# Optimization experiments

Hardware: AMD Instinct MI355X
Metric: run time of the kernel (lower is better)

The kernel has to match this reference:

```python
import jax, jax.numpy as jnp
import numpy as np

ALPHA, BETA, GAMMA = 8.0, 16.0, 16.0  # module defaults


def setup_inputs() -> dict:
    key = jax.random.key(0)
    ks = jax.random.split(key, 8)
    B, T, C = 8, 2048, 128
    d_half, d_rff, lmax, S = 128, 256, 64, 4
    x = jax.random.normal(ks[0], (B, T, C), dtype=jnp.float32)
    # RFF buffers: W ~ N(0,1)/sqrt(c), b ~ U(0, 2pi)
    W = jax.random.normal(ks[1], (C, d_half), dtype=jnp.float32) / np.sqrt(C).astype(np.float32)
    b = 2.0 * np.pi * jax.random.uniform(ks[2], (d_half,), dtype=jnp.float32)
    # phi = Linear(d_rff -> c) + Tanh
    lim = 1.0 / np.sqrt(d_rff)
    phi_w = jax.random.uniform(ks[3], (d_rff, C), minval=-lim, maxval=lim, dtype=jnp.float32)
    phi_b = jax.random.uniform(ks[4], (C,), minval=-lim, maxval=lim, dtype=jnp.float32)
    # anchor is zero-init in torch; use small randn so it contributes
    anchor = 0.02 * jax.random.normal(ks[5], (S, C), dtype=jnp.float32)
    # log-length priors: log_w[s, L-1] = -L / 2^s
    lengths = jnp.arange(1, lmax + 1, dtype=jnp.float32)
    log_w = jnp.stack([-lengths / (2.0 ** s) for s in range(S)])
    lim2 = 1.0 / np.sqrt(S * C)
    mix_w = jax.random.uniform(ks[6], (S * C, C), minval=-lim2, maxval=lim2, dtype=jnp.float32)
    mix_b = jax.random.uniform(ks[7], (C,), minval=-lim2, maxval=lim2, dtype=jnp.float32)
    return {"x": x, "W": W, "b": b, "phi_w": phi_w, "phi_b": phi_b,
            "anchor": anchor, "log_w": log_w, "mix_w": mix_w, "mix_b": mix_b}


def _forward(x, W, b, phi_w, phi_b, anchor, log_w, mix_w, mix_b):
    B, T, C = x.shape
    d_half = W.shape[1]
    d_rff = 2 * d_half
    S, lmax = log_w.shape
    # random Fourier features and causal prefix sums
    z = x @ W + b                                   # (B,T,d_half)
    u = jnp.concatenate([jnp.cos(z), jnp.sin(z)], -1) * (1.0 / np.sqrt(d_half).astype(np.float32))
    pref = jnp.concatenate([jnp.zeros((B, 1, d_rff), x.dtype), jnp.cumsum(u, axis=1)], 1)  # (B,T+1,d)
    # front-pad by lmax so window gathers never go out of bounds
    pref_pad = jnp.concatenate([jnp.zeros((B, lmax, d_rff), x.dtype), pref], 1)            # (B,T+1+lmax,d)

    lengths = jnp.arange(1, lmax + 1, dtype=x.dtype)
    neg_inf = jnp.float32(-jnp.inf)
    # rolling buffers hold states logZ/q/k at indices t-lmax..t-1 (ascending);
    # -inf logZ at out-of-range slots masks invalid segment lengths exactly like L=min(t,lmax)
    logZ0 = jnp.full((S, B, lmax), neg_inf).at[:, :, -1].set(0.0)  # logZ[0]=0
    q0 = jnp.zeros((S, B, lmax, C), x.dtype)
    k0 = jnp.zeros((S, B, lmax), x.dtype)

    @jax.checkpoint
    def step(carry, t):
        logZ_buf, q_buf, k_buf = carry
        # pref[t-lmax .. t]  (pad offset lmax -> start index t)
        sl = jax.lax.dynamic_slice(pref_pad, (0, t, 0), (B, lmax + 1, d_rff))
        # starts = t - lengths, lengths = 1..lmax  -> reversed leading window
        seg_sum = sl[:, -1][:, None, :] - sl[:, :-1][:, ::-1, :]          # (B,lmax,d)
        seg_mean = seg_sum / (lengths + ALPHA)[None, :, None]
        seg_emb = jnp.tanh(seg_mean @ phi_w + phi_b)                      # (B,lmax,C)
        loga = log_w[:, None, :] + logZ_buf[:, :, ::-1]                   # (S,B,lmax)
        pi = jax.nn.softmax(loga, axis=-1)
        q_t = jnp.einsum('sbl,sblc->sbc', pi, q_buf[:, :, ::-1, :] + seg_emb[None])
        k_t = jnp.sum(pi * (k_buf[:, :, ::-1] + 1.0), axis=-1)            # (S,B)
        logZ_t = jax.scipy.special.logsumexp(loga, axis=-1)               # (S,B)
        carry = (jnp.concatenate([logZ_buf[:, :, 1:], logZ_t[:, :, None]], -1),
                 jnp.concatenate([q_buf[:, :, 1:], q_t[:, :, None, :]], 2),
                 jnp.concatenate([k_buf[:, :, 1:], k_t[:, :, None]], -1))
        return carry, (q_t, k_t)

    _, (qs, ks) = jax.lax.scan(step, (logZ0, q0, k0), jnp.arange(1, T + 1))
    # qs: (T,S,B,C), ks: (T,S,B)
    kk = ks[..., None]
    rep = (qs + BETA * anchor[None, :, None, :]) / (kk + BETA) * (kk / (kk + GAMMA))
    h = jnp.transpose(rep, (2, 0, 1, 3)).reshape(B, T, S * C)  # concat scales on feature dim
    return h @ mix_w + mix_b


def reference(x, W, b, phi_w, phi_b, anchor, log_w, mix_w, mix_b):
    return _forward(x, W, b, phi_w, phi_b, anchor, log_w, mix_w, mix_b)
```

## Files before the change

kernel.cpp:

```cpp
#include <hip/hip_runtime.h>
#include <math.h>

#define NB 8
#define NT 2048
#define NC 128
#define NLM 64
#define NS 4
#define QROWS 2049
#define NCH 32

#define TWO_LOG2E 2.885390081777927f
#define LOG2E_F 1.4426950408889634f

__device__ __forceinline__ float rcp_fast(float x) {
  return __builtin_amdgcn_rcpf(x);
}

__device__ __forceinline__ float readlane_f(float v, int lane) {
  return __int_as_float(__builtin_amdgcn_readlane(__float_as_int(v), lane));
}

__device__ __forceinline__ float exp2_fast(float x) {
  float r;
  asm("v_exp_f32 %0, %1" : "=v"(r) : "v"(x));
  return r;
}

__device__ __forceinline__ float fract_fast(float x) {
  float r;
  asm("v_fract_f32 %0, %1" : "=v"(r) : "v"(x));
  return r;
}
__device__ __forceinline__ float sin_rev(float r) {
  float d;
  asm("v_sin_f32 %0, %1" : "=v"(d) : "v"(r));
  return d;
}
__device__ __forceinline__ float cos_rev(float r) {
  float d;
  asm("v_cos_f32 %0, %1" : "=v"(d) : "v"(r));
  return d;
}

template <typename PF, typename DF>
__device__ __forceinline__ void tri_scan64(PF P, DF D, float q[4][16]) {
#pragma unroll
  for (int tau = 0; tau < 4; ++tau) {
    float acc[16];
#pragma unroll
    for (int i = 0; i < 16; ++i) acc[i] = D(tau * 16 + i);
#pragma unroll
    for (int p = 0; p < 4; ++p) {
      if (p < tau) {
#pragma unroll
        for (int i = 0; i < 16; ++i) {
          const int t = tau * 16 + i;
#pragma unroll
          for (int i2 = 0; i2 < 16; ++i2) {
            acc[i] = fmaf(P(t, t - (p * 16 + i2) - 1), q[p][i2], acc[i]);
          }
        }
      }
    }
#pragma unroll
    for (int i = 0; i < 16; ++i) {
      const int t = tau * 16 + i;
#pragma unroll
      for (int i2 = 0; i2 < 16; ++i2) {
        if (i2 < i) acc[i] = fmaf(P(t, i - i2 - 1), q[tau][i2], acc[i]);
      }
      q[tau][i] = acc[i];
    }
  }
}

__global__ __launch_bounds__(256) void k1_uv(
    const float* __restrict__ x, const float* __restrict__ W,
    const float* __restrict__ bias, const float* __restrict__ phiw,
    float* __restrict__ Q) {
  __shared__ __align__(16) float xs[16][128];
  __shared__ float us[16][256];
  const int tid = threadIdx.x;
  const int j = tid & 127;
  const int h = tid >> 7;
  const int r0 = h * 8;
  const int bt0 = blockIdx.x * 16;
  {
    const float4* x4 = (const float4*)(x + (long)bt0 * NC);
    ((float4*)xs)[tid] = x4[tid];
    ((float4*)xs)[tid + 256] = x4[tid + 256];
  }
  __syncthreads();
  float z[8];
  const float bj = bias[j];
#pragma unroll
  for (int r = 0; r < 8; ++r) z[r] = bj;
  for (int k = 0; k < 128; ++k) {
    float w = W[k * 128 + j];
#pragma unroll
    for (int r = 0; r < 8; ++r) z[r] = fmaf(xs[r0 + r][k], w, z[r]);
  }
  const float rs = 0.08838834764831845f;
  const float inv2pi = 0.15915494309189535f;
#pragma unroll
  for (int r = 0; r < 8; ++r) {
    float rf = fract_fast(z[r] * inv2pi);
    us[r0 + r][j] = cos_rev(rf) * rs;
    us[r0 + r][128 + j] = sin_rev(rf) * rs;
  }
  __syncthreads();
  float a[8];
#pragma unroll
  for (int r = 0; r < 8; ++r) a[r] = 0.f;
  for (int k = 0; k < 256; ++k) {
    float w = phiw[k * 128 + j];
#pragma unroll
    for (int r = 0; r < 8; ++r) a[r] = fmaf(us[r0 + r][k], w, a[r]);
  }
#pragma unroll
  for (int r = 0; r < 8; ++r) {
    int bt = bt0 + r0 + r;
    int b = bt >> 11, t = bt & 2047;
    Q[(b * QROWS + t + 1) * NC + j] = a[r];
  }
}

__global__ __launch_bounds__(128) void k23_sums_logz(
    const float* __restrict__ Q, float* __restrict__ S2,
    const float* __restrict__ logw, float* __restrict__ logZt) {
  __shared__ float4 part[4][32];
  __shared__ float wx[64];
  __shared__ float mTs[64][65];
  __shared__ float Zr[64];
  const int x = blockIdx.x;
  const int tid = threadIdx.x;
  if (x < 256) {
    const int b = x >> 5, ch = x & 31;
    const int g = tid >> 5, c4 = tid & 31;
    const float4* Q4 = (const float4*)(Q + (long)(b * QROWS + ch * 64 + 1) * NC);
    float4 acc = make_float4(0.f, 0.f, 0.f, 0.f);
#pragma unroll
    for (int i = 0; i < 16; ++i) {
      float4 v = Q4[(g * 16 + i) * 32 + c4];
      acc.x += v.x; acc.y += v.y; acc.z += v.z; acc.w += v.w;
    }
    part[g][c4] = acc;
    __syncthreads();
    if (g == 0) {
      float4 p0 = part[0][c4], p1 = part[1][c4], p2 = part[2][c4], p3 = part[3][c4];
      ((float4*)(S2 + (long)(b * NCH + ch) * NC))[c4] =
          make_float4(p0.x + p1.x + p2.x + p3.x, p0.y + p1.y + p2.y + p3.y,
                      p0.z + p1.z + p2.z + p3.z, p0.w + p1.w + p2.w + p3.w);
    }
  } else {
    const int s = x - 256;
    const int j = tid;
    if (j < 64) wx[j] = __expf(logw[s * NLM + j]);
    __syncthreads();
    if (j < 64) {
      float q[4][16];
      tri_scan64([&](int t, int l) { return wx[l]; },
                 [&](int t) { int l = t + j; return (l < 64) ? wx[l] : 0.f; }, q);
#pragma unroll
      for (int tau = 0; tau < 4; ++tau)
#pragma unroll
        for (int i = 0; i < 16; ++i) mTs[j][tau * 16 + i] = q[tau][i];
    }
    const int t = j;
    if (t < 64) Zr[t] = (t == 0) ? 1.f : 0.f;
    if (t == 0) logZt[s * QROWS] = 0.f;
    float off = 0.f;
    __syncthreads();
    for (int ch = 0; ch < NCH; ++ch) {
      float acc = 0.f, mx = 0.f;
      if (t < 64) {
#pragma unroll 8
        for (int jj = 0; jj < 64; ++jj) acc = fmaf(mTs[jj][t], Zr[jj], acc);
        logZt[s * QROWS + ch * 64 + 1 + t] = logf(acc) + off;
        mx = acc;
#pragma unroll
        for (int o = 32; o; o >>= 1) mx = fmaxf(mx, __shfl_xor(mx, o));
      }
      __syncthreads();
      if (t < 64) {
        Zr[63 - t] = acc / mx;
        off += logf(mx);
      }
      __syncthreads();
    }
  }
}

__global__ __launch_bounds__(128) void kb_basis_fix(
    const float* __restrict__ logw, const float* __restrict__ logZt,
    float* __restrict__ pig, float* __restrict__ rt, float* __restrict__ ctT,
    float* __restrict__ klocal, float* __restrict__ Q,
    const float* __restrict__ S2) {
  __shared__ __align__(16) float sbuf[16384];
  __shared__ float lzs[128];
  __shared__ float lws[64];
  __shared__ float4 gsum[4][32];
  float* psd = sbuf;
  float* Pts = sbuf + 4096;
  float* Dl = sbuf + 8192;
  float* Rl = sbuf;
  const int x = blockIdx.x;
  const int tid = threadIdx.x;
  if (x < 128) {
    const int s = x >> 5, ch = x & 31;
    {
      int idx = ch * 64 - 63 + tid;
      lzs[tid] = (idx >= 0) ? logZt[s * QROWS + idx] * LOG2E_F : -INFINITY;
      if (tid < 64) lws[tid] = logw[s * NLM + tid] * LOG2E_F;
    }
    __syncthreads();
    {
      const int l = tid & 63, wv = tid >> 6;
      const float lw2 = lws[l];
      for (int tt = wv; tt < 64; tt += 2) {
        float e2 = lw2 + lzs[tt + 63 - l] - lzs[tt + 64];
        float pv = __builtin_exp2f(e2);
        psd[tt * 64 + l] = pv;
        pig[((long)s * NT + ch * 64 + tt) * NLM + l] = pv;
      }
    }
    __syncthreads();
    for (int i = tid; i < 4096; i += 128) {
      int t = i >> 6, tp = i & 63;
      Pts[i] = (tp < t) ? psd[t * 64 + (t - tp - 1)] : 0.f;
    }
    for (int i = tid; i < 8192; i += 128) {
      int t = i >> 7, u = i & 127;
      float d;
      if (u < 64) {
        d = (t == u) ? 1.f : 0.f;
      } else {
        int l = t + (u - 64);
        d = (l < 64) ? psd[t * 64 + l] : 0.f;
      }
      Dl[i] = d;
    }
    __syncthreads();
    float q[4][16];
    const float* Dcol = Dl + tid;
#pragma unroll
    for (int tau = 0; tau < 4; ++tau) {
      float acc[16];
#pragma unroll
      for (int i = 0; i < 16; ++i) acc[i] = Dcol[(tau * 16 + i) * 128];
#pragma unroll
      for (int p = 0; p < 4; ++p) {
        if (p < tau) {
#pragma unroll
          for (int i = 0; i < 16; ++i) {
            const int tr = tau * 16 + i;
            float a = acc[i];
#pragma unroll
            for (int q4 = 0; q4 < 4; ++q4) {
              float4 p4 = *(const float4*)&Pts[tr * 64 + p * 16 + q4 * 4];
              a = fmaf(p4.x, q[p][4 * q4 + 0], a);
              a = fmaf(p4.y, q[p][4 * q4 + 1], a);
              a = fmaf(p4.z, q[p][4 * q4 + 2], a);
              a = fmaf(p4.w, q[p][4 * q4 + 3], a);
            }
            acc[i] = a;
          }
        }
      }
#pragma unroll
      for (int i = 0; i < 16; ++i) {
        const int tr = tau * 16 + i;
        float a = acc[i];
#pragma unroll
        for (int i2 = 0; i2 < 16; ++i2) {
          if (i2 < i) a = fmaf(Pts[tr * 64 + tau * 16 + i2], q[tau][i2], a);
        }
        q[tau][i] = a;
      }
    }
    __syncthreads();
    if (tid < 64) {
      const int tp = tid;
      float* rrow = rt + (((long)s * NCH + ch) * 64 + tp) * 64;
#pragma unroll
      for (int t4 = 0; t4 < 16; ++t4)
        ((float4*)rrow)[t4] = make_float4(
            q[t4 >> 2][4 * (t4 & 3) + 0], q[t4 >> 2][4 * (t4 & 3) + 1],
            q[t4 >> 2][4 * (t4 & 3) + 2], q[t4 >> 2][4 * (t4 & 3) + 3]);
#pragma unroll
      for (int tt = 0; tt < 4; ++tt)
#pragma unroll
        for (int i = 0; i < 16; ++i) Rl[tp * 65 + tt * 16 + i] = q[tt][i];
    } else {
      const int j = tid - 64;
      float* ctb = ctT + ((long)s * NCH + ch) * 4096;
#pragma unroll
      for (int tt = 0; tt < 4; ++tt)
#pragma unroll
        for (int i = 0; i < 16; ++i) ctb[(tt * 16 + i) * 64 + j] = q[tt][i];
    }
    __syncthreads();
    if (tid < 64) {
      float acc = 0.f;
#pragma unroll 8
      for (int tp = 0; tp < 64; ++tp) acc += Rl[tp * 65 + tid];
      klocal[((long)s * NCH + ch) * 64 + tid] = acc;
    }
  } else {
    const int y = x - 128;
    const int b = y >> 5, ch = y & 31;
    const int g = tid >> 5, c4 = tid & 31;
    if (ch == 0 && g == 0)
      ((float4*)(Q + (long)(b * QROWS) * NC))[c4] = make_float4(0.f, 0.f, 0.f, 0.f);
    float4 run = make_float4(0.f, 0.f, 0.f, 0.f);
    for (int i = 0; i < ch; ++i) {
      float4 v = ((const float4*)(S2 + (long)(b * NCH + i) * NC))[c4];
      run.x += v.x; run.y += v.y; run.z += v.z; run.w += v.w;
    }
    float4* Q4 = (float4*)(Q + (long)(b * QROWS + ch * 64 + 1) * NC);
    float4 vbuf[16];
#pragma unroll
    for (int i = 0; i < 16; ++i) vbuf[i] = Q4[(g * 16 + i) * 32 + c4];
    {
      float4 gs = make_float4(0.f, 0.f, 0.f, 0.f);
#pragma unroll
      for (int i = 0; i < 16; ++i) {
        gs.x += vbuf[i].x; gs.y += vbuf[i].y; gs.z += vbuf[i].z; gs.w += vbuf[i].w;
      }
      gsum[g][c4] = gs;
    }
    __syncthreads();
    for (int gp = 0; gp < 3; ++gp) {
      if (gp < g) {
        float4 v = gsum[gp][c4];
        run.x += v.x; run.y += v.y; run.z += v.z; run.w += v.w;
      }
    }
#pragma unroll
    for (int i = 0; i < 16; ++i) {
      run.x += vbuf[i].x; run.y += vbuf[i].y; run.z += vbuf[i].z; run.w += vbuf[i].w;
      Q4[(g * 16 + i) * 32 + c4] = run;
    }
  }
}

__global__ __launch_bounds__(256) void k4_e(
    const float* __restrict__ Q, const float* __restrict__ pi,
    const float* __restrict__ phib, float* __restrict__ eq) {
  __shared__ float Qw[68][64];
  const int b = blockIdx.x;
  const int t0 = blockIdx.y * 4;
  const int half = blockIdx.z;
  const int tid = threadIdx.x;
  for (int i = tid; i < 68 * 64; i += 256) {
    int r = i >> 6, cc = i & 63;
    int tau = t0 - 63 + r;
    Qw[r][cc] = (tau >= 0) ? Q[(b * QROWS + tau) * NC + half * 64 + cc] : 0.f;
  }
  const int c = tid & 63, tg = tid >> 6;
  const int ti = __builtin_amdgcn_readfirstlane(t0 + tg);
  const float* p0 = pi + ((long)0 * NT + ti) * NLM;
  const float* p1 = pi + ((long)1 * NT + ti) * NLM;
  const float* p2 = pi + ((long)2 * NT + ti) * NLM;
  const float* p3 = pi + ((long)3 * NT + ti) * NLM;
  __syncthreads();
  const float pb2 = phib[half * 64 + c] * TWO_LOG2E;
  const float Qt = Qw[tg + 64][c];
  float a0 = 0.f, a1 = 0.f, a2 = 0.f, a3 = 0.f;
#pragma unroll
  for (int lc = 0; lc < 4; ++lc) {
    float v[16];
#pragma unroll
    for (int u = 0; u < 16; ++u) {
      const int l = lc * 16 + u;
      const float cl = TWO_LOG2E / (float)(l + 9);
      float y = (Qt - Qw[tg + 63 - l][c]) * cl + pb2;
      v[u] = rcp_fast(exp2_fast(y) + 1.f);
    }
#pragma unroll
    for (int u = 0; u < 16; ++u) {
      const int l = lc * 16 + u;
      a0 = fmaf(p0[l], v[u], a0);
      a1 = fmaf(p1[l], v[u], a1);
      a2 = fmaf(p2[l], v[u], a2);
      a3 = fmaf(p3[l], v[u], a3);
    }
  }
  const long base = half * 64 + c;
  eq[((long)(0 * 8 + b) * NT + ti) * NC + base] = fmaf(-2.f, a0, 1.f);
  eq[((long)(1 * 8 + b) * NT + ti) * NC + base] = fmaf(-2.f, a1, 1.f);
  eq[((long)(2 * 8 + b) * NT + ti) * NC + base] = fmaf(-2.f, a2, 1.f);
  eq[((long)(3 * 8 + b) * NT + ti) * NC + base] = fmaf(-2.f, a3, 1.f);
}

__global__ __launch_bounds__(128) void k5a_data(const float* __restrict__ rt,
                                                float* __restrict__ eq) {
  __shared__ __align__(16) float rts[4096];
  __shared__ __align__(16) float es[64][128];
  const int sb = blockIdx.x;
  const int s = sb >> 3;
  const int ch = blockIdx.y;
  const int tid = threadIdx.x;
  const float4* rsrc = (const float4*)(rt + ((long)s * NCH + ch) * 4096);
#pragma unroll
  for (int i = 0; i < 8; ++i) ((float4*)rts)[tid + 128 * i] = rsrc[tid + 128 * i];
  float* qb = eq + ((long)sb * NT + ch * 64) * NC;
  const float4* esrc = (const float4*)qb;
#pragma unroll
  for (int i = 0; i < 16; ++i) ((float4*)es)[tid + 128 * i] = esrc[tid + 128 * i];
  __syncthreads();
  const int t0 = (tid >> 4) * 8;
  const int c0 = (tid & 15) * 8;
  float acc[8][8];
#pragma unroll
  for (int i = 0; i < 8; ++i)
#pragma unroll
    for (int k = 0; k < 8; ++k) acc[i][k] = 0.f;
  for (int tp = 0; tp < 64; ++tp) {
    if (tp <= t0 + 7) {
      float4 r0 = *(const float4*)&rts[tp * 64 + t0];
      float4 r1 = *(const float4*)&rts[tp * 64 + t0 + 4];
      float4 e0 = *(const float4*)&es[tp][c0];
      float4 e1 = *(const float4*)&es[tp][c0 + 4];
      float rr[8] = {r0.x, r0.y, r0.z, r0.w, r1.x, r1.y, r1.z, r1.w};
      float ee[8] = {e0.x, e0.y, e0.z, e0.w, e1.x, e1.y, e1.z, e1.w};
#pragma unroll
      for (int i = 0; i < 8; ++i)
#pragma unroll
        for (int k = 0; k < 8; ++k) acc[i][k] = fmaf(rr[i], ee[k], acc[i][k]);
    }
  }
#pragma unroll
  for (int i = 0; i < 8; ++i) {
    float4* dst = (float4*)(qb + (t0 + i) * NC + c0);
    dst[0] = make_float4(acc[i][0], acc[i][1], acc[i][2], acc[i][3]);
    dst[1] = make_float4(acc[i][4], acc[i][5], acc[i][6], acc[i][7]);
  }
}

__global__ __launch_bounds__(256) void k5b_scan(const float* __restrict__ ctT,
                                                const float* __restrict__ klocal,
                                                float* __restrict__ eq,
                                                float* __restrict__ kout) {
  __shared__ float crs[2][64 * 65];
  const int tid = threadIdx.x;
  const int t = tid & 63;
  const int w = tid >> 6;
  const int bid = blockIdx.x;
  const bool isq = bid < 256;
  const int s = isq ? ((bid & 7) >> 1) : (bid - 256);
  const float* ctTs = ctT + (long)s * NCH * 4096;

  const int sr = tid >> 2;
  const int sq = (tid & 3) * 16;
  float4 stg0, stg1, stg2, stg3;

#define K5B_STAGE_LOAD(CH)                                                    \
  {                                                                           \
    const float4* p_ = (const float4*)(ctTs + (CH)*4096 + sr * 64 + sq);      \
    stg0 = p_[0]; stg1 = p_[1]; stg2 = p_[2]; stg3 = p_[3];                   \
  }
#define K5B_STAGE_WRITE(BUF)                                                  \
  {                                                                           \
    float* d_ = &crs[BUF][sr * 65 + sq];                                      \
    d_[0] = stg0.x;  d_[1] = stg0.y;  d_[2] = stg0.z;  d_[3] = stg0.w;        \
    d_[4] = stg1.x;  d_[5] = stg1.y;  d_[6] = stg1.z;  d_[7] = stg1.w;        \
    d_[8] = stg2.x;  d_[9] = stg2.y;  d_[10] = stg2.z; d_[11] = stg2.w;       \
    d_[12] = stg3.x; d_[13] = stg3.y; d_[14] = stg3.z; d_[15] = stg3.w;       \
  }

  const int g = bid >> 3;
  const int bb = g & 7, pp = g >> 3;
  const int hp = bid & 1;
  const int c0 = ((((pp << 1) | hp) << 2) | w) * 4;
  const int sb = s * 8 + bb;
  float* eqb = eq + (long)sb * NT * NC + c0;

  float hv0 = 0.f, hv1 = 0.f, hv2 = 0.f, hv3 = 0.f;
  float hk = 0.f;

  K5B_STAGE_LOAD(0)
  K5B_STAGE_WRITE(0)
  __syncthreads();
#pragma unroll 1
  for (int ch = 0; ch < NCH; ++ch) {
    const int cur = ch & 1;
    if (ch + 1 < NCH) K5B_STAGE_LOAD(ch + 1)
    if (isq) {
      const float* cr = &crs[cur][t * 65];
      float4 ql = *(const float4*)(eqb + (long)(ch * 64 + t) * NC);
      float a0 = 0.f, a1 = 0.f, a2 = 0.f, a3 = 0.f;
#pragma unroll
      for (int j = 0; j < 64; ++j) {
        float cv = cr[j];
        a0 = fmaf(cv, readlane_f(hv0, 63 - j), a0);
        a1 = fmaf(cv, readlane_f(hv1, 63 - j), a1);
        a2 = fmaf(cv, readlane_f(hv2, 63 - j), a2);
        a3 = fmaf(cv, readlane_f(hv3, 63 - j), a3);
      }
      hv0 = a0 + ql.x; hv1 = a1 + ql.y; hv2 = a2 + ql.z; hv3 = a3 + ql.w;
      *(float4*)(eqb + (long)(ch * 64 + t) * NC) =
          make_float4(hv0, hv1, hv2, hv3);
    } else if (tid < 64) {
      const float* cr = &crs[cur][t * 65];
      float acc = klocal[((long)s * NCH + ch) * 64 + t];
#pragma unroll
      for (int j = 0; j < 64; ++j)
        acc = fmaf(cr[j], readlane_f(hk, 63 - j), acc);
      kout[s * NT + ch * 64 + t] = acc;
      hk = acc;
    }
    __syncthreads();
    if (ch + 1 < NCH) K5B_STAGE_WRITE(cur ^ 1)
    __syncthreads();
  }
#undef K5B_STAGE_LOAD
#undef K5B_STAGE_WRITE
}

__global__ __launch_bounds__(256) void k6_mix(
    const float* __restrict__ q, const float* __restrict__ kout,
    const float* __restrict__ anchor, const float* __restrict__ mixw,
    const float* __restrict__ mixb, float* __restrict__ out) {
  __shared__ __align__(16) float rsdata[16][512];
  const int b = blockIdx.x;
  const int t0 = blockIdx.y * 16;
  const int tid = threadIdx.x;
  for (int i = tid; i < 16 * 512; i += 256) {
    int r = i >> 9, sc = i & 511;
    int s = sc >> 7, c = sc & 127;
    int ti = t0 + r;
    float qv = q[((long)(s * 8 + b) * NT + ti) * NC + c];
    float kv = kout[s * NT + ti];
    float d1 = rcp_fast(kv + 16.f);
    rsdata[r][sc] = (qv + 16.f * anchor[sc]) * d1 * (kv * d1);
  }
  __syncthreads();
  const int co = tid & 127, hf = tid >> 7;
  const int r0 = hf * 8;
  float mb = mixb[co];
  float acc[8];
#pragma unroll
  for (int r = 0; r < 8; ++r) acc[r] = mb;
  for (int kk = 0; kk < 512; kk += 4) {
    float wa = mixw[(kk + 0) * 128 + co];
    float wb = mixw[(kk + 1) * 128 + co];
    float wc = mixw[(kk + 2) * 128 + co];
    float wd = mixw[(kk + 3) * 128 + co];
#pragma unroll
    for (int r = 0; r < 8; ++r) {
      float4 rv = *(const float4*)&rsdata[r0 + r][kk];
      acc[r] = fmaf(rv.x, wa, acc[r]);
      acc[r] = fmaf(rv.y, wb, acc[r]);
      acc[r] = fmaf(rv.z, wc, acc[r]);
      acc[r] = fmaf(rv.w, wd, acc[r]);
    }
  }
#pragma unroll
  for (int r = 0; r < 8; ++r)
    out[((long)b * NT + t0 + r0 + r) * NC + co] = acc[r];
}

extern "C" void kernel_launch(void* const* d_in, const int* in_sizes, int n_in,
                              void* d_out, int out_size, void* d_ws, size_t ws_size,
                              hipStream_t stream) {
  const float* x = (const float*)d_in[0];
  const float* W = (const float*)d_in[1];
  const float* bias = (const float*)d_in[2];
  const float* phiw = (const float*)d_in[3];
  const float* phib = (const float*)d_in[4];
  const float* anchor = (const float*)d_in[5];
  const float* logw = (const float*)d_in[6];
  const float* mixw = (const float*)d_in[7];
  const float* mixb = (const float*)d_in[8];
  float* out = (float*)d_out;

  float* ws = (float*)d_ws;
  float* Q = ws;
  float* pi = Q + (long)NB * QROWS * NC;
  float* eq = pi + (long)NS * NT * NLM;
  float* coefTT = eq + (long)NS * NB * NT * NC;
  float* rtb = coefTT + (long)NS * NCH * 4096;
  float* klocal = rtb + (long)NS * NCH * 4096;
  float* kout = klocal + (long)NS * NCH * 64;
  float* logZt = kout + (long)NS * NT;
  float* S2 = logZt + (long)NS * QROWS;

  hipLaunchKernelGGL(k1_uv, dim3(NB * NT / 16), dim3(256), 0, stream, x, W, bias, phiw, Q);
  hipLaunchKernelGGL(k23_sums_logz, dim3(260), dim3(128), 0, stream, Q, S2, logw, logZt);
  hipLaunchKernelGGL(kb_basis_fix, dim3(384), dim3(128), 0, stream, logw, logZt, pi, rtb, coefTT, klocal, Q, S2);
  hipLaunchKernelGGL(k4_e, dim3(NB, NT / 4, 2), dim3(256), 0, stream, Q, pi, phib, eq);
  hipLaunchKernelGGL(k5a_data, dim3(NS * NB, NCH), dim3(128), 0, stream, rtb, eq);
  hipLaunchKernelGGL(k5b_scan, dim3(260), dim3(256), 0, stream, coefTT, klocal, eq, kout);
  hipLaunchKernelGGL(k6_mix, dim3(NB, NT / 16), dim3(256), 0, stream, eq, kout, anchor, mixw, mixb, out);
}
```

Before: 343.7 us.

## Use split-bf16 MFMA for final mixing matmul with pre-transposed weights

Replaces the scalar FP32 FMA loop in the final mixing projection with MFMA 16x16x32 bf16 instructions. Both operands are split into high and low bf16 parts (three MFMAs per k-step) to approximate FP32 accuracy. A new prep kernel transposes and splits mix_w into the reused pi workspace region after k4 has consumed it. This trades some precision and an extra launch for far fewer ALU instructions in k6, which is a small fraction of total time.

```diff
diff --git a/kernel.cpp b/kernel.cpp
--- a/kernel.cpp
+++ b/kernel.cpp
@@ -12,6 +12,9 @@
 #define TWO_LOG2E 2.885390081777927f
 #define LOG2E_F 1.4426950408889634f
 
+typedef __attribute__((__ext_vector_type__(8))) short short8v;
+typedef __attribute__((__ext_vector_type__(4))) float f32x4v;
+
 __device__ __forceinline__ float rcp_fast(float x) {
   return __builtin_amdgcn_rcpf(x);
 }
@@ -40,6 +43,16 @@
   float d;
   asm("v_cos_f32 %0, %1" : "=v"(d) : "v"(r));
   return d;
+}
+
+__device__ __forceinline__ void bf16_split(float v, unsigned short* h,
+                                           unsigned short* l) {
+  unsigned vb = __float_as_uint(v);
+  unsigned short hi = (unsigned short)(vb >> 16);
+  float hf = __uint_as_float((unsigned)hi << 16);
+  float lo = v - hf;
+  *h = hi;
+  *l = (unsigned short)(__float_as_uint(lo) >> 16);
 }
 
 template <typename PF, typename DF>
@@ -393,6 +406,18 @@
   eq[((long)(3 * 8 + b) * NT + ti) * NC + base] = fmaf(-2.f, a3, 1.f);
 }
 
+__global__ __launch_bounds__(256) void k0_prep(
+    const float* __restrict__ mixw, unsigned short* __restrict__ th,
+    unsigned short* __restrict__ tl) {
+  const int i = blockIdx.x * 256 + threadIdx.x;
+  const int k = i >> 7, c = i & 127;
+  float v = mixw[i];
+  unsigned short h, l;
+  bf16_split(v, &h, &l);
+  th[c * 512 + k] = h;
+  tl[c * 512 + k] = l;
+}
+
 __global__ __launch_bounds__(128) void k5a_data(const float* __restrict__ rt,
                                                 float* __restrict__ eq) {
   __shared__ __align__(16) float rts[4096];
@@ -518,47 +543,57 @@
 #undef K5B_STAGE_WRITE
 }
 
-__global__ __launch_bounds__(256) void k6_mix(
+__global__ __launch_bounds__(512) void k6_mix(
     const float* __restrict__ q, const float* __restrict__ kout,
-    const float* __restrict__ anchor, const float* __restrict__ mixw,
+    const float* __restrict__ anchor,
+    const unsigned short* __restrict__ mixwTh,
+    const unsigned short* __restrict__ mixwTl,
     const float* __restrict__ mixb, float* __restrict__ out) {
-  __shared__ __align__(16) float rsdata[16][512];
+  __shared__ unsigned short rsh[16][520];
+  __shared__ unsigned short rsl[16][520];
   const int b = blockIdx.x;
   const int t0 = blockIdx.y * 16;
   const int tid = threadIdx.x;
-  for (int i = tid; i < 16 * 512; i += 256) {
+  for (int i = tid; i < 16 * 512; i += 512) {
     int r = i >> 9, sc = i & 511;
     int s = sc >> 7, c = sc & 127;
     int ti = t0 + r;
     float qv = q[((long)(s * 8 + b) * NT + ti) * NC + c];
     float kv = kout[s * NT + ti];
     float d1 = rcp_fast(kv + 16.f);
-    rsdata[r][sc] = (qv + 16.f * anchor[sc]) * d1 * (kv * d1);
+    float v = (qv + 16.f * anchor[sc]) * d1 * (kv * d1);
+    unsigned short h, l;
+    bf16_split(v, &h, &l);
+    rsh[r][sc] = h;
+    rsl[r][sc] = l;
   }
   __syncthreads();
-  const int co = tid & 127, hf = tid >> 7;
-  const int r0 = hf * 8;
-  float mb = mixb[co];
-  float acc[8];
-#pragma unroll
-  for (int r = 0; r < 8; ++r) acc[r] = mb;
-  for (int kk = 0; kk < 512; kk += 4) {
-    float wa = mixw[(kk + 0) * 128 + co];
-    float wb = mixw[(kk + 1) * 128 + co];
-    float wc = mixw[(kk + 2) * 128 + co];
-    float wd = mixw[(kk + 3) * 128 + co];
-#pragma unroll
-    for (int r = 0; r < 8; ++r) {
-      float4 rv = *(const float4*)&rsdata[r0 + r][kk];
-      acc[r] = fmaf(rv.x, wa, acc[r]);
-      acc[r] = fmaf(rv.y, wb, acc[r]);
-      acc[r] = fmaf(rv.z, wc, acc[r]);
-      acc[r] = fmaf(rv.w, wd, acc[r]);
-    }
-  }
-#pragma unroll
-  for (int r = 0; r < 8; ++r)
-    out[((long)b * NT + t0 + r0 + r) * NC + co] = acc[r];
+  const int w = tid >> 6;
+  const int lane = tid & 63;
+  const int mrow = lane & 15;
+  const int kgrp = lane >> 4;
+  const int c0w = w * 16;
+  const float bias = mixb[c0w + mrow];
+  f32x4v acc = {bias, bias, bias, bias};
+  const unsigned short* bh = mixwTh + (long)(c0w + mrow) * 512 + kgrp * 8;
+  const unsigned short* bl = mixwTl + (long)(c0w + mrow) * 512 + kgrp * 8;
+  const unsigned short* ah = &rsh[mrow][kgrp * 8];
+  const unsigned short* al = &rsl[mrow][kgrp * 8];
+#pragma unroll
+  for (int ks = 0; ks < 16; ++ks) {
+    short8v aH = *(const short8v*)(ah + ks * 32);
+    short8v aL = *(const short8v*)(al + ks * 32);
+    short8v bH = *(const short8v*)(bh + ks * 32);
+    short8v bL = *(const short8v*)(bl + ks * 32);
+    acc = __builtin_amdgcn_mfma_f32_16x16x32_bf16(aH, bH, acc, 0, 0, 0);
+    acc = __builtin_amdgcn_mfma_f32_16x16x32_bf16(aH, bL, acc, 0, 0, 0);
+    acc = __builtin_amdgcn_mfma_f32_16x16x32_bf16(aL, bH, acc, 0, 0, 0);
+  }
+#pragma unroll
+  for (int reg = 0; reg < 4; ++reg) {
+    int row = kgrp * 4 + reg;
+    out[((long)b * NT + t0 + row) * NC + c0w + mrow] = acc[reg];
+  }
 }
 
 extern "C" void kernel_launch(void* const* d_in, const int* in_sizes, int n_in,
@@ -586,11 +621,15 @@
   float* logZt = kout + (long)NS * NT;
   float* S2 = logZt + (long)NS * QROWS;
 
+  unsigned short* mixwTh = (unsigned short*)pi;
+  unsigned short* mixwTl = (unsigned short*)(pi + 32768);
+
   hipLaunchKernelGGL(k1_uv, dim3(NB * NT / 16), dim3(256), 0, stream, x, W, bias, phiw, Q);
   hipLaunchKernelGGL(k23_sums_logz, dim3(260), dim3(128), 0, stream, Q, S2, logw, logZt);
   hipLaunchKernelGGL(kb_basis_fix, dim3(384), dim3(128), 0, stream, logw, logZt, pi, rtb, coefTT, klocal, Q, S2);
   hipLaunchKernelGGL(k4_e, dim3(NB, NT / 4, 2), dim3(256), 0, stream, Q, pi, phib, eq);
+  hipLaunchKernelGGL(k0_prep, dim3(256), dim3(256), 0, stream, mixw, mixwTh, mixwTl);
   hipLaunchKernelGGL(k5a_data, dim3(NS * NB, NCH), dim3(128), 0, stream, rtb, eq);
   hipLaunchKernelGGL(k5b_scan, dim3(260), dim3(256), 0, stream, coefTT, klocal, eq, kout);
-  hipLaunchKernelGGL(k6_mix, dim3(NB, NT / 16), dim3(256), 0, stream, eq, kout, anchor, mixw, mixb, out);
-}
+  hipLaunchKernelGGL(k6_mix, dim3(NB, NT / 16), dim3(512), 0, stream, eq, kout, anchor, mixwTh, mixwTl, mixb, out);
+}
```

After: 331.8 us (median of 3 runs). -3.5%, faster.
